# Kernel optimization log

Hardware: AMD Instinct MI355X
Metric: run time of the kernel (lower is better)

## Reference

```python
import jax, jax.numpy as jnp
import numpy as np
from jax.scipy.special import logsumexp, gammaln

B, T, D, K = 2048, 512, 64, 16  # num_sequences, max_length, data_dim (tones), hidden_dim per factor


def setup_inputs() -> dict:
    key = jax.random.key(0)
    k0, k1, k2, k3, k4 = jax.random.split(key, 5)
    sequences = jax.random.randint(k0, (B, T, D), 0, 2).astype(jnp.int32)  # binary piano-roll obs
    lengths = jax.random.randint(k1, (B,), 1, T + 1).astype(jnp.int32)
    probs_w = jax.nn.softmax(jax.random.normal(k2, (K, K), dtype=jnp.float32), axis=-1)  # row-stochastic
    probs_x = jax.nn.softmax(jax.random.normal(k3, (K, K), dtype=jnp.float32), axis=-1)
    probs_y = jax.random.uniform(k4, (K, K, D), dtype=jnp.float32) * 0.98 + 0.01  # in (0.01, 0.99)
    return {"sequences": sequences, "lengths": lengths,
            "probs_w": probs_w, "probs_x": probs_x, "probs_y": probs_y}


def _dirichlet_logpdf_rows(p, conc):
    # sum over rows of Dirichlet(conc_row).log_prob(p_row)
    return (((conc - 1.0) * jnp.log(p)).sum()
            + gammaln(conc.sum(-1)).sum() - gammaln(conc).sum())


def _log_joint(sequences, lengths, probs_w, probs_x, probs_y):
    dt = probs_y.dtype
    logTw = jnp.log(probs_w)            # (K, K) transition for w factor
    logTx = jnp.log(probs_x)            # (K, K) transition for x factor
    lp = jnp.log(probs_y)               # (K, K, D)
    l1p = jnp.log1p(-probs_y)           # (K, K, D)
    Wemit = (lp - l1p).reshape(K * K, D)        # Bernoulli log-odds per joint state
    base = l1p.sum(-1).reshape(K * K)           # sum_d log(1-p)

    ys = jnp.swapaxes(sequences, 0, 1)          # (T, B, D) int
    mask = jnp.arange(T)[:, None] < lengths[None, :]  # (T, B)

    # alpha[b, w, x]: forward log-prob; initial deterministic state (w, x) = (0, 0)
    alpha0 = jnp.full((B, K, K), -1e9, dtype=dt).at[:, 0, 0].set(0.0)

    def step(alpha, inp):
        y_t, m_t = inp
        y_f = y_t.astype(dt)                                    # (B, D)
        logE = (y_f @ Wemit.T + base).reshape(B, K, K)          # emission log-prob per (w', x')
        # marginalize previous w: (B, x, w')
        tmp = logsumexp(alpha[:, :, :, None] + logTw[None, :, None, :], axis=1)
        # marginalize previous x: (B, w', x')
        new = logsumexp(tmp[:, :, :, None] + logTx[None, :, None, :], axis=1)
        new = new + logE
        alpha = jnp.where(m_t[:, None, None], new, alpha)       # frozen past sequence end
        return alpha, None

    alpha, _ = jax.lax.scan(step, alpha0, (ys, mask))
    seq_ll = logsumexp(alpha.reshape(B, K * K), axis=-1)        # (B,) marginal log-likelihood

    # priors: Dirichlet(0.9*I + 0.1) on transition rows, Beta(0.1, 0.9) on probs_y
    conc = 0.9 * jnp.eye(K, dtype=dt) + 0.1
    prior = _dirichlet_logpdf_rows(probs_w, conc) + _dirichlet_logpdf_rows(probs_x, conc)
    a, b = 0.1, 0.9
    log_beta_norm = gammaln(a) + gammaln(b) - gammaln(a + b)
    prior = prior + ((a - 1.0) * lp + (b - 1.0) * l1p).sum() - log_beta_norm * (K * K * D)

    return seq_ll.sum() + prior


def reference(sequences, lengths, probs_w, probs_x, probs_y):
    return _log_joint(sequences, lengths, probs_w, probs_x, probs_y)
```

## Files before the change

kernel.cpp:

```cpp
#include <hip/hip_runtime.h>
#include <math.h>

#define NB 2048
#define NT 512
#define ND 64

typedef float    f32x4 __attribute__((ext_vector_type(4)));
typedef short    s16x8 __attribute__((ext_vector_type(8)));

#define MFMA32(A,B,C) __builtin_amdgcn_mfma_f32_16x16x32_bf16((A),(B),(C),0,0,0)

#if __has_builtin(__builtin_amdgcn_exp2f)
#define EXP2F(x) __builtin_amdgcn_exp2f(x)
#else
#define EXP2F(x) __expf((x) * 0.6931471805599453f)
#endif
#if __has_builtin(__builtin_amdgcn_logf)
#define LOG2F(x) __builtin_amdgcn_logf(x)
#else
#define LOG2F(x) (__logf(x) * 1.4426950408889634f)
#endif
#if __has_builtin(__builtin_amdgcn_rcpf)
#define RCPF(x) __builtin_amdgcn_rcpf(x)
#else
#define RCPF(x) __fdividef(1.0f, (x))
#endif

__device__ __forceinline__ unsigned short bf16rn(float f) {
  unsigned u = __float_as_uint(f);
  unsigned r = u + 0x7FFFu + ((u >> 16) & 1u);
  return (unsigned short)(r >> 16);
}
__device__ __forceinline__ unsigned pack2(float a, float b) {
  return (unsigned)bf16rn(a) | ((unsigned)bf16rn(b) << 16);
}
__device__ __forceinline__ unsigned pack2t(float a, float b) {
  return (__float_as_uint(a) >> 16) | (__float_as_uint(b) & 0xFFFF0000u);
}

union frag8 { s16x8 s8; unsigned u[4]; };

__device__ __forceinline__ s16x8 pack8t(f32x4 x) {
  frag8 r;
  r.u[0] = pack2t(x[0], x[1]);
  r.u[1] = pack2t(x[2], x[3]);
  r.u[2] = 0u; r.u[3] = 0u;
  return r.s8;
}

__global__ void fhmm_init(const float* __restrict__ py,
                          unsigned short* __restrict__ ws16,
                          float* __restrict__ partials)
{
  const float LOG2E = 1.4426950408889634f;
  int t = blockIdx.x * 256 + threadIdx.x;
  if (t < 2048) partials[t] = 0.f;
  if (t < 2048) {
    int st = t >> 7, kk = (t >> 6) & 1, l = t & 63;
    int rho = st * 16 + (l & 15);
    int s = (4 * (rho >> 6) + (rho & 3)) * 16 + ((rho >> 2) & 15);
    int d0 = kk * 32 + 8 * (l >> 4);
    unsigned short* dst = ws16 + (size_t)t * 8;
#pragma unroll
    for (int i = 0; i < 8; ++i) {
      float p = py[s * 64 + d0 + i];
      dst[i] = bf16rn((logf(p) - log1pf(-p)) * LOG2E);
    }
  } else if (t < 3072) {
    int t2 = t - 2048;
    int st = t2 >> 6, l = t2 & 63;
    unsigned short v[8] = {0, 0, 0, 0, 0, 0, 0, 0};
    if (l < 16) {
      int rho = st * 16 + l;
      int s = (4 * (rho >> 6) + (rho & 3)) * 16 + ((rho >> 2) & 15);
      float base = 0.f;
      for (int d = 0; d < 64; ++d) base += log1pf(-py[s * 64 + d]);
      base *= LOG2E;
      unsigned short hi = bf16rn(base);
      float basehi = __uint_as_float(((unsigned)hi) << 16);
      v[0] = hi;
      v[1] = bf16rn(base - basehi);
    }
    unsigned short* dst = ws16 + (size_t)(2048 + t2) * 8;
#pragma unroll
    for (int i = 0; i < 8; ++i) dst[i] = v[i];
  }
}

__global__ void fhmm_sort(const int* __restrict__ lengths, int* __restrict__ perm)
{
  __shared__ int hist[512];
  __shared__ int cnt[512];
  __shared__ int sa[512], sb2[512];
  const int tid = threadIdx.x;
  hist[tid] = 0; hist[tid + 256] = 0;
  cnt[tid] = 0;  cnt[tid + 256] = 0;
  __syncthreads();
  int myb[8];
#pragma unroll
  for (int u = 0; u < 8; ++u) {
    int i = tid + 256 * u;
    myb[u] = 512 - lengths[i];
    atomicAdd(&hist[myb[u]], 1);
  }
  __syncthreads();
  sa[tid] = hist[tid]; sa[tid + 256] = hist[tid + 256];
  __syncthreads();
  int* src = sa; int* dst = sb2;
  for (int off = 1; off < 512; off <<= 1) {
    for (int k = tid; k < 512; k += 256)
      dst[k] = src[k] + ((k >= off) ? src[k - off] : 0);
    __syncthreads();
    int* tp = src; src = dst; dst = tp;
  }
#pragma unroll
  for (int u = 0; u < 8; ++u) {
    int i = tid + 256 * u;
    int b2 = myb[u];
    int pos = src[b2] - hist[b2] + atomicAdd(&cnt[b2], 1);
    perm[pos] = i;
  }
}

__global__ __launch_bounds__(256, 2) void fhmm_fwd2(
    const int* __restrict__ seq, const int* __restrict__ lengths,
    const float* __restrict__ pw, const float* __restrict__ px,
    const void* __restrict__ wfrag, const int* __restrict__ perm,
    float* __restrict__ partials)
{
  __shared__ f32x4 e_lds[4][1024];

  const int tid = threadIdx.x;
  const int wv = tid >> 6, j = tid & 63;
  const int q = j >> 4, tl = j & 15;
  const int bid = blockIdx.x;
  const int lb  = (bid < 256) ? bid : (767 - bid);
  const int b = perm[(lb << 2) | wv];
  if (b < 0 || b >= NB) return;
  f32x4* e_w = e_lds[wv];
  const s16x8* wf_g = (const s16x8*)wfrag;
  const s16x8* w2_g = wf_g + 2048;

  s16x8 twb8, txb8;
  {
    frag8 a, c;
    a.u[0] = pack2(pw[(4 * q + 0) * 16 + tl], pw[(4 * q + 1) * 16 + tl]);
    a.u[1] = pack2(pw[(4 * q + 2) * 16 + tl], pw[(4 * q + 3) * 16 + tl]);
    a.u[2] = 0u; a.u[3] = 0u;
    c.u[0] = pack2(px[(4 * q + 0) * 16 + tl], px[(4 * q + 1) * 16 + tl]);
    c.u[1] = pack2(px[(4 * q + 2) * 16 + tl], px[(4 * q + 3) * 16 + tl]);
    c.u[2] = 0u; c.u[3] = 0u;
    twb8 = a.s8; txb8 = c.s8;
  }

  s16x8 f2 = {0, 0, 0, 0, 0, 0, 0, 0};
  if (q == 0) { f2[0] = (short)0x3F80; f2[1] = (short)0x3F80; }

  s16x8 ones8;
  {
    frag8 o;
    o.u[0] = 0x3F803F80u; o.u[1] = 0x3F803F80u;
    o.u[2] = 0x3F803F80u; o.u[3] = 0x3F803F80u;
    ones8 = o.s8;
  }

  f32x4 p = {0.f, 0.f, 0.f, 0.f};
  if (j == 0) p[0] = 1.f;

  const int len = lengths[b];
  const int* ybase = seq + (size_t)b * NT * ND;

  int4 ya0, ya1, yb0, yb1;
  {
    const int* yr = ybase + (size_t)tl * ND + 8 * q;
    const int4* pp  = (const int4*)yr;
    const int4* pp2 = (const int4*)(yr + 32);
    ya0 = pp[0]; ya1 = pp[1]; yb0 = pp2[0]; yb1 = pp2[1];
  }

  float L2 = 0.f, Ls = 0.f, R = 0.f;
  const f32x4 z4 = {0.f, 0.f, 0.f, 0.f};

  for (int t0 = 0; t0 < len; t0 += 16) {
    union { s16x8 s; unsigned u[4]; } f0u, f1u;
    f0u.u[0] = (ya0.x ? 0x3F80u : 0u) | (ya0.y ? 0x3F800000u : 0u);
    f0u.u[1] = (ya0.z ? 0x3F80u : 0u) | (ya0.w ? 0x3F800000u : 0u);
    f0u.u[2] = (ya1.x ? 0x3F80u : 0u) | (ya1.y ? 0x3F800000u : 0u);
    f0u.u[3] = (ya1.z ? 0x3F80u : 0u) | (ya1.w ? 0x3F800000u : 0u);
    f1u.u[0] = (yb0.x ? 0x3F80u : 0u) | (yb0.y ? 0x3F800000u : 0u);
    f1u.u[1] = (yb0.z ? 0x3F80u : 0u) | (yb0.w ? 0x3F800000u : 0u);
    f1u.u[2] = (yb1.x ? 0x3F80u : 0u) | (yb1.y ? 0x3F800000u : 0u);
    f1u.u[3] = (yb1.z ? 0x3F80u : 0u) | (yb1.w ? 0x3F800000u : 0u);
    const s16x8 f0 = f0u.s, f1 = f1u.s;

    if (t0 + 16 < len) {
      const int* yr = ybase + (size_t)(t0 + 16 + tl) * ND + 8 * q;
      const int4* pp  = (const int4*)yr;
      const int4* pp2 = (const int4*)(yr + 32);
      ya0 = pp[0]; ya1 = pp[1]; yb0 = pp2[0]; yb1 = pp2[1];
    }

#pragma unroll
    for (int st = 0; st < 16; ++st) {
      f32x4 acc = MFMA32(w2_g[st * 64 + j], f2, z4);
      acc = MFMA32(wf_g[(2 * st + 0) * 64 + j], f0, acc);
      acc = MFMA32(wf_g[(2 * st + 1) * 64 + j], f1, acc);
      f32x4 G;
      G[0] = EXP2F(fminf(acc[0] - R, 80.f));
      G[1] = EXP2F(fminf(acc[1] - R, 80.f));
      G[2] = EXP2F(fminf(acc[2] - R, 80.f));
      G[3] = EXP2F(fminf(acc[3] - R, 80.f));
      e_w[tl * 64 + ((st * 4 + q) ^ tl)] = G;
    }

    const int nsteps = (len - t0 < 16) ? (len - t0) : 16;
    float LsC = 0.f;
    f32x4 gv = e_w[j];
    for (int it = 0; it < nsteps; ++it) {
      const f32x4 g = gv;
      const int itn = (it + 1) & 15;
      gv = e_w[itn * 64 + (j ^ itn)];
      s16x8 vb = pack8t(p);
      f32x4 P  = MFMA32(vb, twb8, z4);
      f32x4 S1 = MFMA32(vb, ones8, z4);
      f32x4 U  = MFMA32(pack8t(P), txb8, z4);
      f32x4 S2 = MFMA32(pack8t(S1), ones8, z4);
      const float s   = fmaxf(S2[0], 1e-30f);
      const float inv = RCPF(s);
      LsC += LOG2F(s);
      f32x4 pn;
      pn[0] = (U[0] * inv) * g[0];
      pn[1] = (U[1] * inv) * g[1];
      pn[2] = (U[2] * inv) * g[2];
      pn[3] = (U[3] * inv) * g[3];
      p = pn;
    }
    L2 += (float)nsteps * R;
    Ls += LsC;
    R  += LsC * 0.0625f;
  }
  {
    f32x4 F1 = MFMA32(pack8t(p), ones8, z4);
    f32x4 F2 = MFMA32(pack8t(F1), ones8, z4);
    float sf = fmaxf(F2[0], 1e-35f);
    float L = (L2 + Ls + LOG2F(sf)) * 0.6931471805599453f;
    if (j == 0) partials[b] = L;
  }
}

__global__ __launch_bounds__(256, 3) void fhmm_fwd1(
    const int* __restrict__ seq, const int* __restrict__ lengths,
    const float* __restrict__ pw, const float* __restrict__ px,
    const float* __restrict__ py, float* __restrict__ partials,
    float* __restrict__ out)
{
  const int b = blockIdx.x, tid = threadIdx.x;
  const int wp = tid >> 4, xc = tid & 15;
  float Twc[16], Txc[16], W[64], base = 0.f;
#pragma unroll
  for (int w = 0; w < 16; ++w) Twc[w] = pw[w * 16 + wp];
#pragma unroll
  for (int x = 0; x < 16; ++x) Txc[x] = px[x * 16 + xc];
#pragma unroll
  for (int d = 0; d < 64; ++d) {
    float pv = py[tid * 64 + d];
    W[d] = logf(pv) - log1pf(-pv);
    base += log1pf(-pv);
  }
  __shared__ __align__(16) float yf[64];
  __shared__ __align__(16) float v_s[256];
  __shared__ __align__(16) float tmp_s[256];
  __shared__ float red[8];
  const int len = lengths[b];
  const int* yb = seq + (size_t)b * (NT * ND);
  v_s[tid] = (tid == 0) ? 1.f : 0.f;
  float L = 0.f, ynext = 0.f;
  if (tid < 64) ynext = (float)yb[tid];
  for (int t = 0; t < len; ++t) {
    if (tid < 64) yf[tid] = ynext;
    __syncthreads();
    if (tid < 64 && (t + 1) < len) ynext = (float)yb[(t + 1) * ND + tid];
    float e0 = base, e1 = 0.f, e2 = 0.f, e3 = 0.f;
    const float4* y4p = (const float4*)yf;
#pragma unroll
    for (int i = 0; i < 16; ++i) {
      float4 y4 = y4p[i];
      e0 = fmaf(y4.x, W[4 * i + 0], e0); e1 = fmaf(y4.y, W[4 * i + 1], e1);
      e2 = fmaf(y4.z, W[4 * i + 2], e2); e3 = fmaf(y4.w, W[4 * i + 3], e3);
    }
    float e = (e0 + e1) + (e2 + e3);
    float s1a = 0.f, s1b = 0.f;
#pragma unroll
    for (int w = 0; w < 16; w += 2) {
      s1a = fmaf(Twc[w], v_s[w * 16 + xc], s1a);
      s1b = fmaf(Twc[w + 1], v_s[(w + 1) * 16 + xc], s1b);
    }
    tmp_s[tid] = s1a + s1b;
    float mm = e;
#pragma unroll
    for (int off = 32; off; off >>= 1) mm = fmaxf(mm, __shfl_xor(mm, off));
    if ((tid & 63) == 0) red[tid >> 6] = mm;
    __syncthreads();
    mm = fmaxf(fmaxf(red[0], red[1]), fmaxf(red[2], red[3]));
    float q0 = 0.f, q1 = 0.f;
    const float4* t4p = (const float4*)(tmp_s + wp * 16);
#pragma unroll
    for (int i = 0; i < 4; ++i) {
      float4 t4 = t4p[i];
      q0 = fmaf(t4.x, Txc[4 * i + 0], q0); q1 = fmaf(t4.y, Txc[4 * i + 1], q1);
      q0 = fmaf(t4.z, Txc[4 * i + 2], q0); q1 = fmaf(t4.w, Txc[4 * i + 3], q1);
    }
    float val = (q0 + q1) * __expf(e - mm);
    float s = val;
#pragma unroll
    for (int off = 32; off; off >>= 1) s += __shfl_xor(s, off);
    if ((tid & 63) == 0) red[4 + (tid >> 6)] = s;
    __syncthreads();
    s = (red[4] + red[5]) + (red[6] + red[7]);
    L += __logf(s) + mm;
    v_s[tid] = val * (1.0f / s);
  }
  if (partials) { if (tid == 0) partials[b] = L; }
  else { if (tid == 0) atomicAdd(out, L); }
}

__global__ void fhmm_finalize(const float* __restrict__ partials,
                              const float* __restrict__ pw,
                              const float* __restrict__ px,
                              const float* __restrict__ py,
                              float* __restrict__ out)
{
  const int tid = threadIdx.x;
  float a = 0.f;
  if (partials) {
#pragma unroll
    for (int i = 0; i < 8; ++i) a += partials[tid + 256 * i];
  }
  {
    int i = tid >> 4, j = tid & 15;
    if (i != j) a += -0.9f * (logf(pw[tid]) + logf(px[tid]));
  }
  for (int k = 0; k < 64; ++k) {
    float p = py[tid * 64 + k];
    a += -0.9f * logf(p) - 0.1f * log1pf(-p);
  }
  __shared__ float red[256];
  red[tid] = a;
  __syncthreads();
  for (int s = 128; s > 0; s >>= 1) {
    if (tid < s) red[tid] += red[tid + s];
    __syncthreads();
  }
  if (tid == 0) {
    const float cst =
        2.f * (16.f * 0.2846828704729192f - 240.f * 2.2527126517342055f)
        - (2.2527126517342055f + 0.0663762397347443f) * 16384.f;
    out[0] = red[0] + cst;
  }
}

extern "C" void kernel_launch(void* const* d_in, const int* in_sizes, int n_in,
                              void* d_out, int out_size, void* d_ws, size_t ws_size,
                              hipStream_t stream) {
  const int*   seq = (const int*)d_in[0];
  const int*   len = (const int*)d_in[1];
  const float* pw  = (const float*)d_in[2];
  const float* px  = (const float*)d_in[3];
  const float* py  = (const float*)d_in[4];
  float*       out = (float*)d_out;

  const size_t NEED = 65536;
  if (ws_size >= NEED) {
    unsigned short* wf = (unsigned short*)d_ws;
    float* partials = (float*)((char*)d_ws + 49152);
    int*   perm     = (int*)((char*)d_ws + 57344);
    fhmm_init<<<12, 256, 0, stream>>>(py, wf, partials);
    fhmm_sort<<<1, 256, 0, stream>>>(len, perm);
    fhmm_fwd2<<<512, 256, 0, stream>>>(seq, len, pw, px, (const void*)wf, perm, partials);
    fhmm_finalize<<<1, 256, 0, stream>>>(partials, pw, px, py, out);
  } else if (ws_size >= 2048 * sizeof(float)) {
    float* partials = (float*)d_ws;
    fhmm_fwd1<<<NB, 256, 0, stream>>>(seq, len, pw, px, py, partials, out);
    fhmm_finalize<<<1, 256, 0, stream>>>(partials, pw, px, py, out);
  } else {
    fhmm_finalize<<<1, 256, 0, stream>>>(nullptr, pw, px, py, out);
    fhmm_fwd1<<<NB, 256, 0, stream>>>(seq, len, pw, px, py, nullptr, out);
  }
}
```

Measured before the change: 206.8 us.

## Factor emission base term out of MFMA and store bf16 emissions in LDS

The per-state base term sum_d log(1-p) is no longer added through an extra MFMA. It is split into a per-wave constant, applied once as len*blen at the end, plus a per-state multiplier gB applied during the recurrence. Emission factors are packed to bf16 pairs in LDS, halving LDS footprint, so blocks grow to 8 waves (512 threads) and the snake-order block mapping is replaced by a contiguous rank mapping. This removes one MFMA per state tile and cuts LDS traffic, at the cost of a bf16 rounding step on emissions and the loss of the length-balancing block order.

```diff
diff --git a/kernel.cpp b/kernel.cpp
--- a/kernel.cpp
+++ b/kernel.cpp
@@ -66,24 +66,12 @@
       float p = py[s * 64 + d0 + i];
       dst[i] = bf16rn((logf(p) - log1pf(-p)) * LOG2E);
     }
-  } else if (t < 3072) {
-    int t2 = t - 2048;
-    int st = t2 >> 6, l = t2 & 63;
-    unsigned short v[8] = {0, 0, 0, 0, 0, 0, 0, 0};
-    if (l < 16) {
-      int rho = st * 16 + l;
-      int s = (4 * (rho >> 6) + (rho & 3)) * 16 + ((rho >> 2) & 15);
-      float base = 0.f;
-      for (int d = 0; d < 64; ++d) base += log1pf(-py[s * 64 + d]);
-      base *= LOG2E;
-      unsigned short hi = bf16rn(base);
-      float basehi = __uint_as_float(((unsigned)hi) << 16);
-      v[0] = hi;
-      v[1] = bf16rn(base - basehi);
-    }
-    unsigned short* dst = ws16 + (size_t)(2048 + t2) * 8;
-#pragma unroll
-    for (int i = 0; i < 8; ++i) dst[i] = v[i];
+  } else if (t < 2304) {
+    int s = t - 2048;
+    float base = 0.f;
+    for (int d = 0; d < 64; ++d) base += log1pf(-py[s * 64 + d]);
+    float* basef = (float*)(ws16 + 16384);
+    basef[s] = base * LOG2E;
   }
 }
 
@@ -122,24 +110,22 @@
   }
 }
 
-__global__ __launch_bounds__(256, 2) void fhmm_fwd2(
+__global__ __launch_bounds__(512, 2) void fhmm_fwd2(
     const int* __restrict__ seq, const int* __restrict__ lengths,
     const float* __restrict__ pw, const float* __restrict__ px,
-    const void* __restrict__ wfrag, const int* __restrict__ perm,
-    float* __restrict__ partials)
-{
-  __shared__ f32x4 e_lds[4][1024];
+    const void* __restrict__ wfrag, const float* __restrict__ basef,
+    const int* __restrict__ perm, float* __restrict__ partials)
+{
+  __shared__ uint2 e_lds[8][1024];
 
   const int tid = threadIdx.x;
   const int wv = tid >> 6, j = tid & 63;
   const int q = j >> 4, tl = j & 15;
-  const int bid = blockIdx.x;
-  const int lb  = (bid < 256) ? bid : (767 - bid);
-  const int b = perm[(lb << 2) | wv];
+  const int rank = (blockIdx.x << 3) | wv;
+  const int b = perm[rank];
   if (b < 0 || b >= NB) return;
-  f32x4* e_w = e_lds[wv];
+  uint2* e_w = e_lds[wv];
   const s16x8* wf_g = (const s16x8*)wfrag;
-  const s16x8* w2_g = wf_g + 2048;
 
   s16x8 twb8, txb8;
   {
@@ -153,15 +139,30 @@
     twb8 = a.s8; txb8 = c.s8;
   }
 
-  s16x8 f2 = {0, 0, 0, 0, 0, 0, 0, 0};
-  if (q == 0) { f2[0] = (short)0x3F80; f2[1] = (short)0x3F80; }
-
   s16x8 ones8;
   {
     frag8 o;
     o.u[0] = 0x3F803F80u; o.u[1] = 0x3F803F80u;
     o.u[2] = 0x3F803F80u; o.u[3] = 0x3F803F80u;
     ones8 = o.s8;
+  }
+
+  f32x4 gB;
+  float blen;
+  {
+    float b0 = basef[(4 * (j >> 4) + 0) * 16 + (j & 15)];
+    float b1 = basef[(4 * (j >> 4) + 1) * 16 + (j & 15)];
+    float b2 = basef[(4 * (j >> 4) + 2) * 16 + (j & 15)];
+    float b3 = basef[(4 * (j >> 4) + 3) * 16 + (j & 15)];
+    float m = (b0 + b1) + (b2 + b3);
+#pragma unroll
+    for (int off = 1; off < 64; off <<= 1) m += __shfl_xor(m, off);
+    const float Rb = m * (1.0f / 256.0f);
+    gB[0] = EXP2F(b0 - Rb);
+    gB[1] = EXP2F(b1 - Rb);
+    gB[2] = EXP2F(b2 - Rb);
+    gB[3] = EXP2F(b3 - Rb);
+    blen = Rb;
   }
 
   f32x4 p = {0.f, 0.f, 0.f, 0.f};
@@ -202,24 +203,27 @@
 
 #pragma unroll
     for (int st = 0; st < 16; ++st) {
-      f32x4 acc = MFMA32(w2_g[st * 64 + j], f2, z4);
-      acc = MFMA32(wf_g[(2 * st + 0) * 64 + j], f0, acc);
+      f32x4 acc = MFMA32(wf_g[(2 * st + 0) * 64 + j], f0, z4);
       acc = MFMA32(wf_g[(2 * st + 1) * 64 + j], f1, acc);
-      f32x4 G;
-      G[0] = EXP2F(fminf(acc[0] - R, 80.f));
-      G[1] = EXP2F(fminf(acc[1] - R, 80.f));
-      G[2] = EXP2F(fminf(acc[2] - R, 80.f));
-      G[3] = EXP2F(fminf(acc[3] - R, 80.f));
-      e_w[tl * 64 + ((st * 4 + q) ^ tl)] = G;
+      float G0 = EXP2F(fminf(acc[0] - R, 80.f));
+      float G1 = EXP2F(fminf(acc[1] - R, 80.f));
+      float G2 = EXP2F(fminf(acc[2] - R, 80.f));
+      float G3 = EXP2F(fminf(acc[3] - R, 80.f));
+      e_w[tl * 64 + ((st * 4 + q) ^ tl)] = make_uint2(pack2t(G0, G1), pack2t(G2, G3));
     }
 
     const int nsteps = (len - t0 < 16) ? (len - t0) : 16;
     float LsC = 0.f;
-    f32x4 gv = e_w[j];
+    uint2 ev = e_w[j];
     for (int it = 0; it < nsteps; ++it) {
-      const f32x4 g = gv;
+      const uint2 ec = ev;
       const int itn = (it + 1) & 15;
-      gv = e_w[itn * 64 + (j ^ itn)];
+      ev = e_w[itn * 64 + (j ^ itn)];
+      f32x4 hv;
+      hv[0] = __uint_as_float(ec.x << 16)        * gB[0];
+      hv[1] = __uint_as_float(ec.x & 0xFFFF0000u) * gB[1];
+      hv[2] = __uint_as_float(ec.y << 16)        * gB[2];
+      hv[3] = __uint_as_float(ec.y & 0xFFFF0000u) * gB[3];
       s16x8 vb = pack8t(p);
       f32x4 P  = MFMA32(vb, twb8, z4);
       f32x4 S1 = MFMA32(vb, ones8, z4);
@@ -229,10 +233,10 @@
       const float inv = RCPF(s);
       LsC += LOG2F(s);
       f32x4 pn;
-      pn[0] = (U[0] * inv) * g[0];
-      pn[1] = (U[1] * inv) * g[1];
-      pn[2] = (U[2] * inv) * g[2];
-      pn[3] = (U[3] * inv) * g[3];
+      pn[0] = (U[0] * inv) * hv[0];
+      pn[1] = (U[1] * inv) * hv[1];
+      pn[2] = (U[2] * inv) * hv[2];
+      pn[3] = (U[3] * inv) * hv[3];
       p = pn;
     }
     L2 += (float)nsteps * R;
@@ -243,7 +247,7 @@
     f32x4 F1 = MFMA32(pack8t(p), ones8, z4);
     f32x4 F2 = MFMA32(pack8t(F1), ones8, z4);
     float sf = fmaxf(F2[0], 1e-35f);
-    float L = (L2 + Ls + LOG2F(sf)) * 0.6931471805599453f;
+    float L = (L2 + Ls + (float)len * blen + LOG2F(sf)) * 0.6931471805599453f;
     if (j == 0) partials[b] = L;
   }
 }
@@ -372,11 +376,13 @@
   const size_t NEED = 65536;
   if (ws_size >= NEED) {
     unsigned short* wf = (unsigned short*)d_ws;
+    const float* basef = (const float*)((char*)d_ws + 32768);
     float* partials = (float*)((char*)d_ws + 49152);
     int*   perm     = (int*)((char*)d_ws + 57344);
     fhmm_init<<<12, 256, 0, stream>>>(py, wf, partials);
     fhmm_sort<<<1, 256, 0, stream>>>(len, perm);
-    fhmm_fwd2<<<512, 256, 0, stream>>>(seq, len, pw, px, (const void*)wf, perm, partials);
+    fhmm_fwd2<<<256, 512, 0, stream>>>(seq, len, pw, px, (const void*)wf,
+                                       basef, perm, partials);
     fhmm_finalize<<<1, 256, 0, stream>>>(partials, pw, px, py, out);
   } else if (ws_size >= 2048 * sizeof(float)) {
     float* partials = (float*)d_ws;
```

Result: slower. 218.2 us (+5.5%).

## Store emission factors as bf16 in LDS, unroll full 16-step chunks, remap blocks

Applied to the files above, without the earlier changes.

Emission factors are packed as bf16 pairs in LDS, halving shared memory per wave and the bytes read in the serial recurrence. Full 16-step chunks get a fully unrolled path with a two-deep LDS prefetch, while partial chunks keep the loop. The block-to-sorted-bucket mapping also changes from a mirrored order to an interleaved one, altering load balance. The emission factors lose precision before the multiply, though the recurrence already rounds to bf16 for the MFMA inputs.

```diff
diff --git a/kernel.cpp b/kernel.cpp
--- a/kernel.cpp
+++ b/kernel.cpp
@@ -128,16 +128,16 @@
     const void* __restrict__ wfrag, const int* __restrict__ perm,
     float* __restrict__ partials)
 {
-  __shared__ f32x4 e_lds[4][1024];
+  __shared__ uint2 e_lds[4][1024];
 
   const int tid = threadIdx.x;
   const int wv = tid >> 6, j = tid & 63;
   const int q = j >> 4, tl = j & 15;
   const int bid = blockIdx.x;
-  const int lb  = (bid < 256) ? bid : (767 - bid);
+  const int lb  = (bid < 256) ? (2 * bid) : (2 * (bid - 256) + 1);
   const int b = perm[(lb << 2) | wv];
   if (b < 0 || b >= NB) return;
-  f32x4* e_w = e_lds[wv];
+  uint2* e_w = e_lds[wv];
   const s16x8* wf_g = (const s16x8*)wfrag;
   const s16x8* w2_g = wf_g + 2048;
 
@@ -205,35 +205,70 @@
       f32x4 acc = MFMA32(w2_g[st * 64 + j], f2, z4);
       acc = MFMA32(wf_g[(2 * st + 0) * 64 + j], f0, acc);
       acc = MFMA32(wf_g[(2 * st + 1) * 64 + j], f1, acc);
-      f32x4 G;
-      G[0] = EXP2F(fminf(acc[0] - R, 80.f));
-      G[1] = EXP2F(fminf(acc[1] - R, 80.f));
-      G[2] = EXP2F(fminf(acc[2] - R, 80.f));
-      G[3] = EXP2F(fminf(acc[3] - R, 80.f));
-      e_w[tl * 64 + ((st * 4 + q) ^ tl)] = G;
+      float G0 = EXP2F(fminf(acc[0] - R, 80.f));
+      float G1 = EXP2F(fminf(acc[1] - R, 80.f));
+      float G2 = EXP2F(fminf(acc[2] - R, 80.f));
+      float G3 = EXP2F(fminf(acc[3] - R, 80.f));
+      e_w[tl * 64 + ((st * 4 + q) ^ tl)] = make_uint2(pack2t(G0, G1), pack2t(G2, G3));
     }
 
     const int nsteps = (len - t0 < 16) ? (len - t0) : 16;
     float LsC = 0.f;
-    f32x4 gv = e_w[j];
-    for (int it = 0; it < nsteps; ++it) {
-      const f32x4 g = gv;
-      const int itn = (it + 1) & 15;
-      gv = e_w[itn * 64 + (j ^ itn)];
-      s16x8 vb = pack8t(p);
-      f32x4 P  = MFMA32(vb, twb8, z4);
-      f32x4 S1 = MFMA32(vb, ones8, z4);
-      f32x4 U  = MFMA32(pack8t(P), txb8, z4);
-      f32x4 S2 = MFMA32(pack8t(S1), ones8, z4);
-      const float s   = fmaxf(S2[0], 1e-30f);
-      const float inv = RCPF(s);
-      LsC += LOG2F(s);
-      f32x4 pn;
-      pn[0] = (U[0] * inv) * g[0];
-      pn[1] = (U[1] * inv) * g[1];
-      pn[2] = (U[2] * inv) * g[2];
-      pn[3] = (U[3] * inv) * g[3];
-      p = pn;
+    if (nsteps == 16) {
+      uint2 ga = e_w[j];
+      uint2 gb = e_w[64 + (j ^ 1)];
+#define FSTEP(IT)                                                          \
+      {                                                                    \
+        const uint2 ec = ga; ga = gb;                                      \
+        if ((IT) < 14)                                                     \
+          gb = e_w[(((IT) + 2) & 15) * 64 + (j ^ (((IT) + 2) & 15))];      \
+        f32x4 hv;                                                          \
+        hv[0] = __uint_as_float(ec.x << 16);                               \
+        hv[1] = __uint_as_float(ec.x & 0xFFFF0000u);                       \
+        hv[2] = __uint_as_float(ec.y << 16);                               \
+        hv[3] = __uint_as_float(ec.y & 0xFFFF0000u);                       \
+        s16x8 vb = pack8t(p);                                              \
+        f32x4 P  = MFMA32(vb, twb8, z4);                                   \
+        f32x4 S1 = MFMA32(vb, ones8, z4);                                  \
+        f32x4 U  = MFMA32(pack8t(P), txb8, z4);                            \
+        f32x4 S2 = MFMA32(pack8t(S1), ones8, z4);                          \
+        const float s   = fmaxf(S2[0], 1e-30f);                            \
+        const float inv = RCPF(s);                                         \
+        LsC += LOG2F(s);                                                   \
+        p[0] = (U[0] * inv) * hv[0];                                       \
+        p[1] = (U[1] * inv) * hv[1];                                       \
+        p[2] = (U[2] * inv) * hv[2];                                       \
+        p[3] = (U[3] * inv) * hv[3];                                       \
+      }
+      FSTEP(0)  FSTEP(1)  FSTEP(2)  FSTEP(3)
+      FSTEP(4)  FSTEP(5)  FSTEP(6)  FSTEP(7)
+      FSTEP(8)  FSTEP(9)  FSTEP(10) FSTEP(11)
+      FSTEP(12) FSTEP(13) FSTEP(14) FSTEP(15)
+#undef FSTEP
+    } else {
+      uint2 ev = e_w[j];
+      for (int it = 0; it < nsteps; ++it) {
+        const uint2 ec = ev;
+        const int itn = (it + 1) & 15;
+        ev = e_w[itn * 64 + (j ^ itn)];
+        f32x4 hv;
+        hv[0] = __uint_as_float(ec.x << 16);
+        hv[1] = __uint_as_float(ec.x & 0xFFFF0000u);
+        hv[2] = __uint_as_float(ec.y << 16);
+        hv[3] = __uint_as_float(ec.y & 0xFFFF0000u);
+        s16x8 vb = pack8t(p);
+        f32x4 P  = MFMA32(vb, twb8, z4);
+        f32x4 S1 = MFMA32(vb, ones8, z4);
+        f32x4 U  = MFMA32(pack8t(P), txb8, z4);
+        f32x4 S2 = MFMA32(pack8t(S1), ones8, z4);
+        const float s   = fmaxf(S2[0], 1e-30f);
+        const float inv = RCPF(s);
+        LsC += LOG2F(s);
+        p[0] = (U[0] * inv) * hv[0];
+        p[1] = (U[1] * inv) * hv[1];
+        p[2] = (U[2] * inv) * hv[2];
+        p[3] = (U[3] * inv) * hv[3];
+      }
     }
     L2 += (float)nsteps * R;
     Ls += LsC;
```

Result: slower. 284.7 us (+37.6%).

## Software-pipeline emission computation with forward recursion using double-buffered bf16 LDS

Applied to the files above, without the earlier changes.

Emission exponentials for the next 16-step chunk are now computed and interleaved into the serial forward recursion of the current chunk, writing into a second LDS buffer. The goal is to hide the latency-bound dependent MFMA chain behind independent emission MFMAs and exps. Emissions are stored packed as bf16 to halve LDS footprint for the double buffer. The cost is precision loss in emission factors and a one-chunk-lagged rescaling offset, plus more register pressure from full unrolling.

```diff
diff --git a/kernel.cpp b/kernel.cpp
--- a/kernel.cpp
+++ b/kernel.cpp
@@ -128,7 +128,7 @@
     const void* __restrict__ wfrag, const int* __restrict__ perm,
     float* __restrict__ partials)
 {
-  __shared__ f32x4 e_lds[4][1024];
+  __shared__ uint2 e_lds[4][2][1024];
 
   const int tid = threadIdx.x;
   const int wv = tid >> 6, j = tid & 63;
@@ -137,7 +137,8 @@
   const int lb  = (bid < 256) ? bid : (767 - bid);
   const int b = perm[(lb << 2) | wv];
   if (b < 0 || b >= NB) return;
-  f32x4* e_w = e_lds[wv];
+  uint2* ea = e_lds[wv][0];
+  uint2* eb = e_lds[wv][1];
   const s16x8* wf_g = (const s16x8*)wfrag;
   const s16x8* w2_g = wf_g + 2048;
 
@@ -169,75 +170,107 @@
 
   const int len = lengths[b];
   const int* ybase = seq + (size_t)b * NT * ND;
+  const f32x4 z4 = {0.f, 0.f, 0.f, 0.f};
 
   int4 ya0, ya1, yb0, yb1;
+  s16x8 f0, f1;
+
+#define LOADY(ROWBASE)                                                     \
+  {                                                                        \
+    int row_ = (ROWBASE) + tl;                                             \
+    if (row_ > len - 1) row_ = len - 1;     \
+    const int* yr = ybase + (size_t)row_ * ND + 8 * q;                     \
+    const int4* pp  = (const int4*)yr;                                     \
+    const int4* pp2 = (const int4*)(yr + 32);                              \
+    ya0 = pp[0]; ya1 = pp[1]; yb0 = pp2[0]; yb1 = pp2[1];                  \
+  }
+
+#define BUILDF01                                                           \
+  {                                                                        \
+    frag8 f0u_, f1u_;                                                      \
+    f0u_.u[0] = (ya0.x ? 0x3F80u : 0u) | (ya0.y ? 0x3F800000u : 0u);       \
+    f0u_.u[1] = (ya0.z ? 0x3F80u : 0u) | (ya0.w ? 0x3F800000u : 0u);       \
+    f0u_.u[2] = (ya1.x ? 0x3F80u : 0u) | (ya1.y ? 0x3F800000u : 0u);       \
+    f0u_.u[3] = (ya1.z ? 0x3F80u : 0u) | (ya1.w ? 0x3F800000u : 0u);       \
+    f1u_.u[0] = (yb0.x ? 0x3F80u : 0u) | (yb0.y ? 0x3F800000u : 0u);       \
+    f1u_.u[1] = (yb0.z ? 0x3F80u : 0u) | (yb0.w ? 0x3F800000u : 0u);       \
+    f1u_.u[2] = (yb1.x ? 0x3F80u : 0u) | (yb1.y ? 0x3F800000u : 0u);       \
+    f1u_.u[3] = (yb1.z ? 0x3F80u : 0u) | (yb1.w ? 0x3F800000u : 0u);       \
+    f0 = f0u_.s8; f1 = f1u_.s8;                                            \
+  }
+
+#define EMIT_ST(ST, EO, RN)                                                \
+  {                                                                        \
+    f32x4 acc_ = MFMA32(w2_g[(ST) * 64 + j], f2, z4);                      \
+    acc_ = MFMA32(wf_g[(2 * (ST) + 0) * 64 + j], f0, acc_);                \
+    acc_ = MFMA32(wf_g[(2 * (ST) + 1) * 64 + j], f1, acc_);                \
+    float G0_ = EXP2F(fminf(acc_[0] - (RN), 80.f));                        \
+    float G1_ = EXP2F(fminf(acc_[1] - (RN), 80.f));                        \
+    float G2_ = EXP2F(fminf(acc_[2] - (RN), 80.f));                        \
+    float G3_ = EXP2F(fminf(acc_[3] - (RN), 80.f));                        \
+    (EO)[tl * 64 + (((ST) * 4 + q) ^ tl)] =                                \
+        make_uint2(pack2t(G0_, G1_), pack2t(G2_, G3_));                    \
+  }
+
+#define FSTEP_I(IT, ECUR)                                                  \
+  {                                                                        \
+    const uint2 ec_ = ev;                                                  \
+    const int itn_ = ((IT) + 1) & 15;                                      \
+    ev = (ECUR)[itn_ * 64 + (j ^ itn_)];                                   \
+    f32x4 hv_;                                                             \
+    hv_[0] = __uint_as_float(ec_.x << 16);                                 \
+    hv_[1] = __uint_as_float(ec_.x & 0xFFFF0000u);                         \
+    hv_[2] = __uint_as_float(ec_.y << 16);                                 \
+    hv_[3] = __uint_as_float(ec_.y & 0xFFFF0000u);                         \
+    s16x8 vb_ = pack8t(p);                                                 \
+    f32x4 P_  = MFMA32(vb_, twb8, z4);                                     \
+    f32x4 S1_ = MFMA32(vb_, ones8, z4);                                    \
+    f32x4 U_  = MFMA32(pack8t(P_), txb8, z4);                              \
+    f32x4 S2_ = MFMA32(pack8t(S1_), ones8, z4);                            \
+    const float s_   = fmaxf(S2_[0], 1e-30f);                              \
+    const float inv_ = RCPF(s_);                                           \
+    LsC += LOG2F(s_);                                                      \
+    p[0] = (U_[0] * inv_) * hv_[0];                                        \
+    p[1] = (U_[1] * inv_) * hv_[1];                                        \
+    p[2] = (U_[2] * inv_) * hv_[2];                                        \
+    p[3] = (U_[3] * inv_) * hv_[3];                                        \
+  }
+
+  LOADY(0)
+  BUILDF01
+#pragma unroll
+  for (int st = 0; st < 16; ++st) EMIT_ST(st, ea, 0.f)
+
+  float L2 = 0.f, Ls = 0.f, Rcur = 0.f, Rfb = 0.f;
+  if (16 < len) LOADY(16)
+
+  int t0 = 0;
+  while (t0 + 16 < len) {
+    BUILDF01
+    if (t0 + 32 < len) LOADY(t0 + 32)
+    const float Rn = Rfb;
+    float LsC = 0.f;
+    uint2 ev = ea[j];
+#define ISTEP(IT) { FSTEP_I(IT, ea) EMIT_ST(IT, eb, Rn) }
+    ISTEP(0)  ISTEP(1)  ISTEP(2)  ISTEP(3)
+    ISTEP(4)  ISTEP(5)  ISTEP(6)  ISTEP(7)
+    ISTEP(8)  ISTEP(9)  ISTEP(10) ISTEP(11)
+    ISTEP(12) ISTEP(13) ISTEP(14) ISTEP(15)
+#undef ISTEP
+    L2 += 16.f * Rcur;
+    Ls += LsC;
+    Rfb += LsC * 0.0625f;
+    Rcur = Rn;
+    { uint2* tp = ea; ea = eb; eb = tp; }
+    t0 += 16;
+  }
   {
-    const int* yr = ybase + (size_t)tl * ND + 8 * q;
-    const int4* pp  = (const int4*)yr;
-    const int4* pp2 = (const int4*)(yr + 32);
-    ya0 = pp[0]; ya1 = pp[1]; yb0 = pp2[0]; yb1 = pp2[1];
-  }
-
-  float L2 = 0.f, Ls = 0.f, R = 0.f;
-  const f32x4 z4 = {0.f, 0.f, 0.f, 0.f};
-
-  for (int t0 = 0; t0 < len; t0 += 16) {
-    union { s16x8 s; unsigned u[4]; } f0u, f1u;
-    f0u.u[0] = (ya0.x ? 0x3F80u : 0u) | (ya0.y ? 0x3F800000u : 0u);
-    f0u.u[1] = (ya0.z ? 0x3F80u : 0u) | (ya0.w ? 0x3F800000u : 0u);
-    f0u.u[2] = (ya1.x ? 0x3F80u : 0u) | (ya1.y ? 0x3F800000u : 0u);
-    f0u.u[3] = (ya1.z ? 0x3F80u : 0u) | (ya1.w ? 0x3F800000u : 0u);
-    f1u.u[0] = (yb0.x ? 0x3F80u : 0u) | (yb0.y ? 0x3F800000u : 0u);
-    f1u.u[1] = (yb0.z ? 0x3F80u : 0u) | (yb0.w ? 0x3F800000u : 0u);
-    f1u.u[2] = (yb1.x ? 0x3F80u : 0u) | (yb1.y ? 0x3F800000u : 0u);
-    f1u.u[3] = (yb1.z ? 0x3F80u : 0u) | (yb1.w ? 0x3F800000u : 0u);
-    const s16x8 f0 = f0u.s, f1 = f1u.s;
-
-    if (t0 + 16 < len) {
-      const int* yr = ybase + (size_t)(t0 + 16 + tl) * ND + 8 * q;
-      const int4* pp  = (const int4*)yr;
-      const int4* pp2 = (const int4*)(yr + 32);
-      ya0 = pp[0]; ya1 = pp[1]; yb0 = pp2[0]; yb1 = pp2[1];
-    }
-
-#pragma unroll
-    for (int st = 0; st < 16; ++st) {
-      f32x4 acc = MFMA32(w2_g[st * 64 + j], f2, z4);
-      acc = MFMA32(wf_g[(2 * st + 0) * 64 + j], f0, acc);
-      acc = MFMA32(wf_g[(2 * st + 1) * 64 + j], f1, acc);
-      f32x4 G;
-      G[0] = EXP2F(fminf(acc[0] - R, 80.f));
-      G[1] = EXP2F(fminf(acc[1] - R, 80.f));
-      G[2] = EXP2F(fminf(acc[2] - R, 80.f));
-      G[3] = EXP2F(fminf(acc[3] - R, 80.f));
-      e_w[tl * 64 + ((st * 4 + q) ^ tl)] = G;
-    }
-
-    const int nsteps = (len - t0 < 16) ? (len - t0) : 16;
+    const int nst = len - t0;
     float LsC = 0.f;
-    f32x4 gv = e_w[j];
-    for (int it = 0; it < nsteps; ++it) {
-      const f32x4 g = gv;
-      const int itn = (it + 1) & 15;
-      gv = e_w[itn * 64 + (j ^ itn)];
-      s16x8 vb = pack8t(p);
-      f32x4 P  = MFMA32(vb, twb8, z4);
-      f32x4 S1 = MFMA32(vb, ones8, z4);
-      f32x4 U  = MFMA32(pack8t(P), txb8, z4);
-      f32x4 S2 = MFMA32(pack8t(S1), ones8, z4);
-      const float s   = fmaxf(S2[0], 1e-30f);
-      const float inv = RCPF(s);
-      LsC += LOG2F(s);
-      f32x4 pn;
-      pn[0] = (U[0] * inv) * g[0];
-      pn[1] = (U[1] * inv) * g[1];
-      pn[2] = (U[2] * inv) * g[2];
-      pn[3] = (U[3] * inv) * g[3];
-      p = pn;
-    }
-    L2 += (float)nsteps * R;
+    uint2 ev = ea[j];
+    for (int it = 0; it < nst; ++it) FSTEP_I(it, ea)
+    L2 += (float)nst * Rcur;
     Ls += LsC;
-    R  += LsC * 0.0625f;
   }
   {
     f32x4 F1 = MFMA32(pack8t(p), ones8, z4);
@@ -246,6 +279,10 @@
     float L = (L2 + Ls + LOG2F(sf)) * 0.6931471805599453f;
     if (j == 0) partials[b] = L;
   }
+#undef LOADY
+#undef BUILDF01
+#undef EMIT_ST
+#undef FSTEP_I
 }
 
 __global__ __launch_bounds__(256, 3) void fhmm_fwd1(
```

After: 213.4 us. 1.03x slower.
